# Kernel optimization log

Measured on AMD Instinct MI355X. Metric: run time of the kernel, lower is better.

## Reference

```python
import jax, jax.numpy as jnp
import numpy as np

B, S, D_MODEL, H = 4, 2048, 1024, 16
D_K = D_MODEL // H


def setup_inputs() -> dict:
    key = jax.random.key(0)
    kx, kq, kk, kv, ko = jax.random.split(key, 5)
    scale = 1.0 / np.sqrt(D_MODEL)
    return {
        "x": jax.random.normal(kx, (B, S, D_MODEL), dtype=jnp.float32),
        "W_q": jax.random.normal(kq, (D_MODEL, D_MODEL), dtype=jnp.float32) * scale,
        "W_k": jax.random.normal(kk, (D_MODEL, D_MODEL), dtype=jnp.float32) * scale,
        "W_v": jax.random.normal(kv, (D_MODEL, D_MODEL), dtype=jnp.float32) * scale,
        "W_out": jax.random.normal(ko, (D_MODEL, D_MODEL), dtype=jnp.float32) * scale,
    }


def reference(x, W_q, W_k, W_v, W_out):
    # nn.Linear(bias=False): y = x @ W.T; weights stored as (out, in).
    Bx, Sx, D = x.shape
    q = (x @ W_q.T).reshape(Bx, Sx, H, D_K).transpose(0, 2, 1, 3)  # (B,H,S,d_k)
    k = (x @ W_k.T).reshape(Bx, Sx, H, D_K).transpose(0, 2, 1, 3)
    v = (x @ W_v.T).reshape(Bx, Sx, H, D_K).transpose(0, 2, 1, 3)
    scores = jnp.einsum("bhsd,bhtd->bhst", q, k) / jnp.sqrt(jnp.float32(D_K))
    attn = jax.nn.softmax(scores, axis=-1)
    out = jnp.einsum("bhst,bhtd->bhsd", attn, v)  # (B,H,S,d_k)
    out = out.transpose(0, 2, 1, 3).reshape(Bx, Sx, D)  # combine heads
    return out @ W_out.T
```

## Files before the change

### kernel.cpp

```cpp
#include <hip/hip_runtime.h>

#define BATCH 4
#define SEQ 2048
#define DM 1024
#define NH 16
#define DK 64

typedef unsigned short u16;
typedef unsigned int u32;
typedef __attribute__((ext_vector_type(8))) short bfrag;
typedef __attribute__((ext_vector_type(4))) short bfrag4;
typedef __attribute__((ext_vector_type(4))) float ffrag;

__device__ inline u16 f2bf(float f) {
  union { float f; u32 u; } v; v.f = f;
  u32 u = v.u;
  return (u16)((u + 0x7FFFu + ((u >> 16) & 1u)) >> 16);
}
__device__ inline float bf2f(u16 u) {
  union { u32 u; float f; } v; v.u = ((u32)u) << 16;
  return v.f;
}
__device__ inline ffrag MFMA(bfrag a, bfrag b, ffrag c) {
  return __builtin_amdgcn_mfma_f32_16x16x32_bf16(a, b, c, 0, 0, 0);
}
#if defined(__has_builtin)
#if __has_builtin(__builtin_amdgcn_mfma_f32_16x16x16bf16_1k)
#define HAVE_MFMA16 1
#endif
#endif
#if HAVE_MFMA16
__device__ inline ffrag MFMA16(bfrag4 a, bfrag4 b, ffrag c) {
  return __builtin_amdgcn_mfma_f32_16x16x16bf16_1k(a, b, c, 0, 0, 0);
}
#else
__device__ inline ffrag MFMA16(bfrag4 a, bfrag4 b, ffrag c) { return c; }
#endif

__device__ __forceinline__ void g2l16(const u16* g, u16* l) {
  __builtin_amdgcn_global_load_lds(
      (const __attribute__((address_space(1))) u16*)g,
      (__attribute__((address_space(3))) u16*)l, 16, 0, 0);
}

__global__ __launch_bounds__(256) void cvt_bf16(const float* __restrict__ in,
                                                u16* __restrict__ out, int n4) {
  int i = blockIdx.x * 256 + threadIdx.x;
  if (i >= n4) return;
  float4 v = ((const float4*)in)[i];
  union { u16 u[4]; uint2 d; } o;
  o.u[0] = f2bf(v.x); o.u[1] = f2bf(v.y); o.u[2] = f2bf(v.z); o.u[3] = f2bf(v.w);
  ((uint2*)out)[i] = o.d;
}

__global__ __launch_bounds__(256) void cvt_w4(
    const float* __restrict__ a, const float* __restrict__ b,
    const float* __restrict__ c, const float* __restrict__ d,
    u16* __restrict__ oa, u16* __restrict__ ob,
    u16* __restrict__ oc, u16* __restrict__ od) {
  int which = blockIdx.x >> 10;
  int i = (blockIdx.x & 1023) * 256 + threadIdx.x;
  const float* in = which == 0 ? a : which == 1 ? b : which == 2 ? c : d;
  u16* out = which == 0 ? oa : which == 1 ? ob : which == 2 ? oc : od;
  float4 v = ((const float4*)in)[i];
  union { u16 u[4]; uint2 dd; } o;
  o.u[0] = f2bf(v.x); o.u[1] = f2bf(v.y); o.u[2] = f2bf(v.z); o.u[3] = f2bf(v.w);
  ((uint2*)out)[i] = o.dd;
}

__global__ __launch_bounds__(256) void gemm_qkv(
    const u16* __restrict__ xb,
    const u16* __restrict__ Wq, const u16* __restrict__ Wk,
    const u16* __restrict__ Wv,
    u16* __restrict__ Qb, u16* __restrict__ Ksw, u16* __restrict__ Vsw) {
  const int z = blockIdx.z;
  const u16* Bm = z == 0 ? Wq : z == 1 ? Wk : Wv;

  const int K = DM;
  const int bm = blockIdx.y * 128, bn = blockIdx.x * 128;
  __shared__ __align__(16) u16 As[128 * 32];
  __shared__ __align__(16) u16 Bs[128 * 32];
  const int tid = threadIdx.x;
  const int lane = tid & 63;
  const int w = tid >> 6;
  const int wr = w >> 1, wc = w & 1;
  const int l15 = lane & 15, quad = lane >> 4;
  const int srow = tid >> 2, scol = (tid & 3) * 8;

  ffrag acc[4][4] = {};

  for (int k0 = 0; k0 < K; k0 += 32) {
    __syncthreads();
    g2l16(&xb[(size_t)(bm + srow) * K + k0 + scol], &As[tid * 8]);
    g2l16(&xb[(size_t)(bm + 64 + srow) * K + k0 + scol], &As[(tid + 256) * 8]);
    g2l16(&Bm[(size_t)(bn + srow) * K + k0 + scol], &Bs[tid * 8]);
    g2l16(&Bm[(size_t)(bn + 64 + srow) * K + k0 + scol], &Bs[(tid + 256) * 8]);
    __syncthreads();
    bfrag af[4], bf[4];
    if (z < 2) {
#pragma unroll
      for (int i = 0; i < 4; i++)
        af[i] = *(const bfrag*)(&As[(wr * 64 + i * 16 + l15) * 32 + quad * 8]);
#pragma unroll
      for (int j = 0; j < 4; j++)
        bf[j] = *(const bfrag*)(&Bs[(wc * 64 + j * 16 + l15) * 32 + quad * 8]);
    } else {
#pragma unroll
      for (int i = 0; i < 4; i++)
        af[i] = *(const bfrag*)(&Bs[(wr * 64 + i * 16 + l15) * 32 + quad * 8]);
#pragma unroll
      for (int j = 0; j < 4; j++)
        bf[j] = *(const bfrag*)(&As[(wc * 64 + j * 16 + l15) * 32 + quad * 8]);
    }
#pragma unroll
    for (int i = 0; i < 4; i++)
#pragma unroll
      for (int j = 0; j < 4; j++)
        acc[i][j] = MFMA(af[i], bf[j], acc[i][j]);
  }

  if (z == 0) {
#pragma unroll
    for (int i = 0; i < 4; i++)
#pragma unroll
      for (int j = 0; j < 4; j++)
#pragma unroll
        for (int r = 0; r < 4; r++) {
          int m = bm + wr * 64 + i * 16 + quad * 4 + r;
          int n = bn + wc * 64 + j * 16 + l15;
          int b = m >> 11, s = m & 2047;
          int h = n >> 6, d = n & 63;
          Qb[(((size_t)(b * NH + h)) * SEQ + s) * DK + d] = f2bf(acc[i][j][r]);
        }
  } else if (z == 1) {
#pragma unroll
    for (int i = 0; i < 4; i++)
#pragma unroll
      for (int j = 0; j < 4; j++)
#pragma unroll
        for (int r = 0; r < 4; r++) {
          int m = bm + wr * 64 + i * 16 + quad * 4 + r;
          int n = bn + wc * 64 + j * 16 + l15;
          int b = m >> 11, s = m & 2047;
          int h = n >> 6, d = n & 63;
          size_t hb = (size_t)(b * NH + h) * (SEQ * DK);
          size_t off = hb + (size_t)(s >> 6) * 4096 +
              ((((s >> 4) & 3) * 2 + (d >> 5)) * 64 +
               ((d >> 3) & 3) * 16 + (s & 15)) * 8 + (d & 7);
          Ksw[off] = f2bf(acc[i][j][r]);
        }
  } else {
#pragma unroll
    for (int i = 0; i < 4; i++)
#pragma unroll
      for (int j = 0; j < 4; j++)
#pragma unroll
        for (int r = 0; r < 4; r++) {
          int n = bn + wr * 64 + i * 16 + quad * 4 + r;
          int m = bm + wc * 64 + j * 16 + l15;
          int b = m >> 11, s = m & 2047;
          int h = n >> 6, d = n & 63;
          size_t hb = (size_t)(b * NH + h) * (SEQ * DK);
          size_t off = hb + (size_t)(s >> 6) * 4096 +
              ((((d >> 4) * 4 + ((s >> 4) & 3)) * 64 +
                ((s >> 2) & 3) * 16 + (d & 15)) * 4 + (s & 3));
          Vsw[off] = f2bf(acc[i][j][r]);
        }
  }
}

__global__ __launch_bounds__(256) void gemm_out(
    const u16* __restrict__ Ab, const u16* __restrict__ Wo, float* __restrict__ C) {
  const int K = DM, N = DM;
  const int bm = blockIdx.y * 128, bn = blockIdx.x * 128;
  __shared__ __align__(16) u16 As[128 * 32];
  __shared__ __align__(16) u16 Bs[128 * 32];
  const int tid = threadIdx.x;
  const int lane = tid & 63;
  const int w = tid >> 6;
  const int wr = w >> 1, wc = w & 1;
  const int l15 = lane & 15, quad = lane >> 4;
  const int srow = tid >> 2, scol = (tid & 3) * 8;

  ffrag acc[4][4] = {};

  for (int k0 = 0; k0 < K; k0 += 32) {
    __syncthreads();
    g2l16(&Ab[(size_t)(bm + srow) * K + k0 + scol], &As[tid * 8]);
    g2l16(&Ab[(size_t)(bm + 64 + srow) * K + k0 + scol], &As[(tid + 256) * 8]);
    g2l16(&Wo[(size_t)(bn + srow) * K + k0 + scol], &Bs[tid * 8]);
    g2l16(&Wo[(size_t)(bn + 64 + srow) * K + k0 + scol], &Bs[(tid + 256) * 8]);
    __syncthreads();
    bfrag af[4], bf[4];
#pragma unroll
    for (int i = 0; i < 4; i++)
      af[i] = *(const bfrag*)(&As[(wr * 64 + i * 16 + l15) * 32 + quad * 8]);
#pragma unroll
    for (int j = 0; j < 4; j++)
      bf[j] = *(const bfrag*)(&Bs[(wc * 64 + j * 16 + l15) * 32 + quad * 8]);
#pragma unroll
    for (int i = 0; i < 4; i++)
#pragma unroll
      for (int j = 0; j < 4; j++)
        acc[i][j] = MFMA(af[i], bf[j], acc[i][j]);
  }

#pragma unroll
  for (int i = 0; i < 4; i++)
#pragma unroll
    for (int j = 0; j < 4; j++)
#pragma unroll
      for (int r = 0; r < 4; r++) {
        int m = bm + wr * 64 + i * 16 + quad * 4 + r;
        int n = bn + wc * 64 + j * 16 + l15;
        C[(size_t)m * N + n] = acc[i][j][r];
      }
}

__global__ __launch_bounds__(256) void attn(
    const u16* __restrict__ Qb, const u16* __restrict__ Ksw,
    const u16* __restrict__ Vsw, u16* __restrict__ Ab) {
  const int bh = blockIdx.y;
  const int b = bh >> 4, h = bh & 15;
  const int qbase = blockIdx.x * 128;
  const int tid = threadIdx.x;
  const int w = tid >> 6, lane = tid & 63;
  const int l15 = lane & 15, quad = lane >> 4;

  __shared__ __align__(16) u16 Kt[2][4096];
  __shared__ __align__(16) u16 Vt[2][4096];

  const size_t hbase = (size_t)bh * SEQ * DK;

  const float qscale = 0.125f * 1.4426950408889634f;
  bfrag q[2][2];
#pragma unroll
  for (int i = 0; i < 2; i++)
#pragma unroll
    for (int kk = 0; kk < 2; kk++) {
      bfrag t = *(const bfrag*)(&Qb[hbase +
          (size_t)(qbase + w * 32 + i * 16 + l15) * DK + kk * 32 + quad * 8]);
#pragma unroll
      for (int e = 0; e < 8; e++)
        q[i][kk][e] = (short)f2bf(bf2f((u16)t[e]) * qscale);
    }

  ffrag O[4][2] = {};
  float lsum[2] = {0.f, 0.f};

  {
    const u16* ks = &Ksw[hbase];
    const u16* vs = &Vsw[hbase];
    g2l16(&ks[tid * 8], &Kt[0][tid * 8]);
    g2l16(&ks[2048 + tid * 8], &Kt[0][2048 + tid * 8]);
    g2l16(&vs[tid * 8], &Vt[0][tid * 8]);
    g2l16(&vs[2048 + tid * 8], &Vt[0][2048 + tid * 8]);
  }

  for (int t = 0; t < SEQ / 64; t++) {
    const int buf = t & 1;
    __syncthreads();
    if (t + 1 < SEQ / 64) {
      const u16* ks = &Ksw[hbase + (size_t)(t + 1) * 4096];
      const u16* vs = &Vsw[hbase + (size_t)(t + 1) * 4096];
      g2l16(&ks[tid * 8], &Kt[buf ^ 1][tid * 8]);
      g2l16(&ks[2048 + tid * 8], &Kt[buf ^ 1][2048 + tid * 8]);
      g2l16(&vs[tid * 8], &Vt[buf ^ 1][tid * 8]);
      g2l16(&vs[2048 + tid * 8], &Vt[buf ^ 1][2048 + tid * 8]);
    }

    bfrag4 pb[4][2];
#pragma unroll
    for (int j = 0; j < 4; j++) {
      bfrag k0f = *(const bfrag*)(&Kt[buf][((j * 2 + 0) * 64 + lane) * 8]);
      bfrag k1f = *(const bfrag*)(&Kt[buf][((j * 2 + 1) * 64 + lane) * 8]);
#pragma unroll
      for (int i = 0; i < 2; i++) {
        ffrag z = {};
        z = MFMA(k0f, q[i][0], z);
        z = MFMA(k1f, q[i][1], z);
        u32 u[4]; float ts = 0.f;
#pragma unroll
        for (int r = 0; r < 4; r++) {
          float p = __builtin_amdgcn_exp2f(z[r]);
          u[r] = __float_as_uint(p);
          ts += __uint_as_float(u[r] & 0xffff0000u);
        }
        lsum[i] += ts;
        union { u32 d[2]; bfrag4 v; } pk;
        pk.d[0] = (u[1] & 0xffff0000u) | (u[0] >> 16);
        pk.d[1] = (u[3] & 0xffff0000u) | (u[2] >> 16);
        pb[j][i] = pk.v;
      }
    }

#pragma unroll
    for (int j = 0; j < 4; j++)
#pragma unroll
      for (int db = 0; db < 4; db++) {
        bfrag4 vf = *(const bfrag4*)(&Vt[buf][((db * 4 + j) * 64 + lane) * 4]);
        O[db][0] = MFMA16(vf, pb[j][0], O[db][0]);
        O[db][1] = MFMA16(vf, pb[j][1], O[db][1]);
      }
  }

  float rl[2];
#pragma unroll
  for (int i = 0; i < 2; i++) {
    float s = lsum[i];
    s += __shfl_xor(s, 16);
    s += __shfl_xor(s, 32);
    rl[i] = 1.0f / s;
  }

  const size_t obase = ((size_t)b * SEQ) * DM + (size_t)h * DK;
#pragma unroll
  for (int db = 0; db < 4; db++)
#pragma unroll
    for (int i = 0; i < 2; i++) {
      int s = qbase + w * 32 + i * 16 + l15;
      union { u16 u[4]; uint2 d; } o;
#pragma unroll
      for (int r = 0; r < 4; r++) o.u[r] = f2bf(O[db][i][r] * rl[i]);
      *(uint2*)(&Ab[obase + (size_t)s * DM + db * 16 + quad * 4]) = o.d;
    }
}

extern "C" void kernel_launch(void* const* d_in, const int* in_sizes, int n_in,
                              void* d_out, int out_size, void* d_ws, size_t ws_size,
                              hipStream_t stream) {
  const float* x  = (const float*)d_in[0];
  const float* Wq = (const float*)d_in[1];
  const float* Wk = (const float*)d_in[2];
  const float* Wv = (const float*)d_in[3];
  const float* Wo = (const float*)d_in[4];
  float* out = (float*)d_out;

  char* ws = (char*)d_ws;
  u16* xb  = (u16*)(ws + 0);
  u16* Wqb = (u16*)(ws + 16777216);
  u16* Wkb = (u16*)(ws + 18874368);
  u16* Wvb = (u16*)(ws + 20971520);
  u16* Wob = (u16*)(ws + 23068672);
  u16* Qb  = (u16*)(ws + 25165824);
  u16* Ksw = (u16*)(ws + 41943040);
  u16* Vsw = (u16*)(ws + 58720256);
  u16* Ab  = (u16*)(ws + 75497472);
  const size_t NEED = 92274688;
  if (ws_size < NEED) return;

  cvt_bf16<<<8192, 256, 0, stream>>>(x, xb, (BATCH * SEQ * DM) / 4);
  cvt_w4<<<4096, 256, 0, stream>>>(Wq, Wk, Wv, Wo, Wqb, Wkb, Wvb, Wob);

  dim3 gqkv(DM / 128, (BATCH * SEQ) / 128, 3);
  gemm_qkv<<<gqkv, 256, 0, stream>>>(xb, Wqb, Wkb, Wvb, Qb, Ksw, Vsw);

  dim3 gat(SEQ / 128, BATCH * NH);
  attn<<<gat, 256, 0, stream>>>(Qb, Ksw, Vsw, Ab);

  dim3 gout(DM / 128, (BATCH * SEQ) / 128);
  gemm_out<<<gout, 256, 0, stream>>>(Ab, Wob, out);
}
```

Measured before the change: 299.5 us.

## Fold softmax scale into W_q, stage QKV epilogue via LDS, MFMA row sums

Folds the 1/sqrt(d_k)*log2(e) factor into the bf16 conversion of W_q, so the attention kernel loads Q fragments directly with no per-element rescale. The QKV GEMM epilogue now writes each wave's tile into shared memory in the target swizzled layout, then copies it to global memory with 16-byte stores instead of scattered 2-byte stores. In attention, the per-lane row-sum accumulation and shuffle reduction are replaced by an MFMA against a ones vector, and bf16 packing uses a byte-permute instruction. Rounding Q once after scaling the weights changes numerics slightly, and the epilogue adds barriers and shared-memory round trips.

```diff
diff --git a/kernel.cpp b/kernel.cpp
--- a/kernel.cpp
+++ b/kernel.cpp
@@ -16,10 +16,6 @@
   union { float f; u32 u; } v; v.f = f;
   u32 u = v.u;
   return (u16)((u + 0x7FFFu + ((u >> 16) & 1u)) >> 16);
-}
-__device__ inline float bf2f(u16 u) {
-  union { u32 u; float f; } v; v.u = ((u32)u) << 16;
-  return v.f;
 }
 __device__ inline ffrag MFMA(bfrag a, bfrag b, ffrag c) {
   return __builtin_amdgcn_mfma_f32_16x16x32_bf16(a, b, c, 0, 0, 0);
@@ -62,9 +58,11 @@
   int i = (blockIdx.x & 1023) * 256 + threadIdx.x;
   const float* in = which == 0 ? a : which == 1 ? b : which == 2 ? c : d;
   u16* out = which == 0 ? oa : which == 1 ? ob : which == 2 ? oc : od;
+  float sc = (which == 0) ? 0.18033688011112042f : 1.0f;
   float4 v = ((const float4*)in)[i];
   union { u16 u[4]; uint2 dd; } o;
-  o.u[0] = f2bf(v.x); o.u[1] = f2bf(v.y); o.u[2] = f2bf(v.z); o.u[3] = f2bf(v.w);
+  o.u[0] = f2bf(v.x * sc); o.u[1] = f2bf(v.y * sc);
+  o.u[2] = f2bf(v.z * sc); o.u[3] = f2bf(v.w * sc);
   ((uint2*)out)[i] = o.dd;
 }
 
@@ -119,53 +117,52 @@
         acc[i][j] = MFMA(af[i], bf[j], acc[i][j]);
   }
 
-  if (z == 0) {
-#pragma unroll
-    for (int i = 0; i < 4; i++)
-#pragma unroll
-      for (int j = 0; j < 4; j++)
-#pragma unroll
-        for (int r = 0; r < 4; r++) {
-          int m = bm + wr * 64 + i * 16 + quad * 4 + r;
-          int n = bn + wc * 64 + j * 16 + l15;
-          int b = m >> 11, s = m & 2047;
-          int h = n >> 6, d = n & 63;
-          Qb[(((size_t)(b * NH + h)) * SEQ + s) * DK + d] = f2bf(acc[i][j][r]);
-        }
-  } else if (z == 1) {
-#pragma unroll
-    for (int i = 0; i < 4; i++)
-#pragma unroll
-      for (int j = 0; j < 4; j++)
-#pragma unroll
-        for (int r = 0; r < 4; r++) {
-          int m = bm + wr * 64 + i * 16 + quad * 4 + r;
-          int n = bn + wc * 64 + j * 16 + l15;
-          int b = m >> 11, s = m & 2047;
-          int h = n >> 6, d = n & 63;
-          size_t hb = (size_t)(b * NH + h) * (SEQ * DK);
-          size_t off = hb + (size_t)(s >> 6) * 4096 +
-              ((((s >> 4) & 3) * 2 + (d >> 5)) * 64 +
-               ((d >> 3) & 3) * 16 + (s & 15)) * 8 + (d & 7);
-          Ksw[off] = f2bf(acc[i][j][r]);
-        }
-  } else {
-#pragma unroll
-    for (int i = 0; i < 4; i++)
-#pragma unroll
-      for (int j = 0; j < 4; j++)
-#pragma unroll
-        for (int r = 0; r < 4; r++) {
-          int n = bn + wr * 64 + i * 16 + quad * 4 + r;
-          int m = bm + wc * 64 + j * 16 + l15;
-          int b = m >> 11, s = m & 2047;
-          int h = n >> 6, d = n & 63;
-          size_t hb = (size_t)(b * NH + h) * (SEQ * DK);
-          size_t off = hb + (size_t)(s >> 6) * 4096 +
-              ((((d >> 4) * 4 + ((s >> 4) & 3)) * 64 +
-                ((s >> 2) & 3) * 16 + (d & 15)) * 4 + (s & 3));
-          Vsw[off] = f2bf(acc[i][j][r]);
-        }
+  __syncthreads();
+  u16* img = (w & 1) ? Bs : As;
+  const int tokbase = (z == 2) ? (bm + wc * 64) : (bm + wr * 64);
+  const int nbase   = (z == 2) ? (bn + wr * 64) : (bn + wc * 64);
+  const int bb = tokbase >> 11, s0 = tokbase & 2047, h = nbase >> 6;
+  u16* gp;
+  if (z == 0) gp = Qb + (((size_t)(bb * NH + h)) * SEQ + s0) * DK;
+  else gp = (z == 1 ? Ksw : Vsw) + (size_t)(bb * NH + h) * (SEQ * DK) +
+            (size_t)(s0 >> 6) * 4096;
+
+  for (int pass = 0; pass < 2; pass++) {
+    if ((w >> 1) == pass) {
+      if (z == 0) {
+#pragma unroll
+        for (int i = 0; i < 4; i++)
+#pragma unroll
+          for (int j = 0; j < 4; j++)
+#pragma unroll
+            for (int r = 0; r < 4; r++)
+              img[(i * 16 + quad * 4 + r) * 64 + j * 16 + l15] = f2bf(acc[i][j][r]);
+      } else if (z == 1) {
+#pragma unroll
+        for (int i = 0; i < 4; i++)
+#pragma unroll
+          for (int j = 0; j < 4; j++)
+#pragma unroll
+            for (int r = 0; r < 4; r++)
+              img[((i * 2 + (j >> 1)) * 64 + ((j & 1) * 2 + (l15 >> 3)) * 16 +
+                   quad * 4 + r) * 8 + (l15 & 7)] = f2bf(acc[i][j][r]);
+      } else {
+#pragma unroll
+        for (int i = 0; i < 4; i++)
+#pragma unroll
+          for (int j = 0; j < 4; j++)
+#pragma unroll
+            for (int r = 0; r < 4; r++)
+              img[((i * 4 + j) * 64 + (l15 >> 2) * 16 + quad * 4 + r) * 4 +
+                  (l15 & 3)] = f2bf(acc[i][j][r]);
+      }
+#pragma unroll
+      for (int c = 0; c < 8; c++) {
+        int idx = (c * 64 + lane) * 8;
+        *(int4*)(&gp[idx]) = *(const int4*)(&img[idx]);
+      }
+    }
+    if (pass == 0) __syncthreads();
   }
 }
 
@@ -232,21 +229,17 @@
 
   const size_t hbase = (size_t)bh * SEQ * DK;
 
-  const float qscale = 0.125f * 1.4426950408889634f;
   bfrag q[2][2];
 #pragma unroll
   for (int i = 0; i < 2; i++)
 #pragma unroll
-    for (int kk = 0; kk < 2; kk++) {
-      bfrag t = *(const bfrag*)(&Qb[hbase +
+    for (int kk = 0; kk < 2; kk++)
+      q[i][kk] = *(const bfrag*)(&Qb[hbase +
           (size_t)(qbase + w * 32 + i * 16 + l15) * DK + kk * 32 + quad * 8]);
-#pragma unroll
-      for (int e = 0; e < 8; e++)
-        q[i][kk][e] = (short)f2bf(bf2f((u16)t[e]) * qscale);
-    }
-
+
+  const bfrag4 ones = {(short)0x3F80, (short)0x3F80, (short)0x3F80, (short)0x3F80};
   ffrag O[4][2] = {};
-  float lsum[2] = {0.f, 0.f};
+  ffrag Lacc[2] = {};
 
   {
     const u16* ks = &Ksw[hbase];
@@ -279,18 +272,15 @@
         ffrag z = {};
         z = MFMA(k0f, q[i][0], z);
         z = MFMA(k1f, q[i][1], z);
-        u32 u[4]; float ts = 0.f;
-#pragma unroll
-        for (int r = 0; r < 4; r++) {
-          float p = __builtin_amdgcn_exp2f(z[r]);
-          u[r] = __float_as_uint(p);
-          ts += __uint_as_float(u[r] & 0xffff0000u);
-        }
-        lsum[i] += ts;
+        u32 u[4];
+#pragma unroll
+        for (int r = 0; r < 4; r++)
+          u[r] = __float_as_uint(__builtin_amdgcn_exp2f(z[r]));
         union { u32 d[2]; bfrag4 v; } pk;
-        pk.d[0] = (u[1] & 0xffff0000u) | (u[0] >> 16);
-        pk.d[1] = (u[3] & 0xffff0000u) | (u[2] >> 16);
+        pk.d[0] = __builtin_amdgcn_perm(u[1], u[0], 0x07060302u);
+        pk.d[1] = __builtin_amdgcn_perm(u[3], u[2], 0x07060302u);
         pb[j][i] = pk.v;
+        Lacc[i] = MFMA16(ones, pk.v, Lacc[i]);
       }
     }
 
@@ -304,14 +294,7 @@
       }
   }
 
-  float rl[2];
-#pragma unroll
-  for (int i = 0; i < 2; i++) {
-    float s = lsum[i];
-    s += __shfl_xor(s, 16);
-    s += __shfl_xor(s, 32);
-    rl[i] = 1.0f / s;
-  }
+  float rl[2] = {1.0f / Lacc[0][0], 1.0f / Lacc[1][0]};
 
   const size_t obase = ((size_t)b * SEQ) * DM + (size_t)h * DK;
 #pragma unroll
```

After: 307.4 us. +2.6%, slower.
